# Kernel tuning notes

Measured on AMD Instinct MI355X. Metric: run time of the kernel, lower is better.

Reference implementation:

```python
import jax, jax.numpy as jnp
import numpy as np

M_SIZE = 128          # local window half-size
SCALING = 1.0 / np.sqrt(64.0)


def _window_allowed(seq_len, m):
    """Boolean [L, L] mask; True where attention is allowed.

    Matches torch window_mask: window width = 2m+1; rows near the edges are
    clamped so every row sees exactly `2m+1` columns.
    """
    size = 2 * m + 1
    if seq_len <= size:
        return jnp.ones((seq_len, seq_len), dtype=bool)
    rows = jnp.arange(seq_len)[:, None]            # [L,1]
    cols = jnp.arange(seq_len)[None, :]            # [1,L]
    start = jnp.clip(rows - m, 0, seq_len - size)  # [L,1]
    return (cols >= start) & (cols < start + size)


def setup_inputs() -> dict:
    key = jax.random.key(0)
    kq, kk, kv = jax.random.split(key, 3)
    B, L, D = 8, 4096, 64
    q = jax.random.normal(kq, (B, L, D), dtype=jnp.float32)
    k = jax.random.normal(kk, (B, L, D), dtype=jnp.float32)
    v = jax.random.normal(kv, (B, L, D), dtype=jnp.float32)
    return {"q": q, "k": k, "v": v}


def reference(q, k, v):
    # scores: [B, Lq, Lk]
    scores = jnp.einsum("bqd,bkd->bqk", q, k) * SCALING
    allowed = _window_allowed(q.shape[1], M_SIZE)          # [L, L]
    scores = jnp.where(allowed[None, :, :], scores, -jnp.inf)
    attention = jax.nn.softmax(scores, axis=2)
    out = jnp.einsum("bqk,bkv->bqv", attention, v)
    return (out, attention)
```

## Files before the change

### kernel.cpp

```cpp
#include <hip/hip_runtime.h>
#include <math.h>

#define L_SEQ 4096
#define D_HEAD 64
#define M_WIN 128
#define WIN 257
#define QB 8
#define W 264
#define WF4 66
#define ATTS 272
#define SCALE 0.125f

#define RL(v, i) __uint_as_float(__builtin_amdgcn_readlane(__float_as_uint(v), (i)))

static __device__ __forceinline__ unsigned bfr(float x) {
    unsigned u = __float_as_uint(x);
    return (u + 0x7fffu + ((u >> 16) & 1u)) >> 16;
}
static __device__ __forceinline__ unsigned bfpack(float lo, float hi) {
    return bfr(lo) | (bfr(hi) << 16);
}

__global__ __launch_bounds__(256, 3) void win_attn_kernel(
    const float* __restrict__ Q, const float* __restrict__ K,
    const float* __restrict__ V, float* __restrict__ OutO,
    float* __restrict__ OutA)
{
    extern __shared__ float smem[];
    uint4* k_su = (uint4*)smem;
    float* att  = smem + 2112 * 4;

    const int t  = threadIdx.x;
    const int w  = t >> 6;
    const int ln = t & 63;

    const int bid = (blockIdx.x & 7) * 512 + (blockIdx.x >> 3);
    const int b   = bid >> 9;
    const int q0  = (bid & 511) * QB;

    int s0 = q0 - M_WIN;
    if (s0 < 0) s0 = 0;
    if (s0 > L_SEQ - WIN) s0 = L_SEQ - WIN;
    const int wcount = (L_SEQ - s0 < W) ? (L_SEQ - s0) : W;

    {
        const float4* Kg = (const float4*)(K + ((size_t)(b * L_SEQ + s0)) * D_HEAD);
        #pragma unroll 3
        for (int idx = t; idx < 264 * 8; idx += 256) {
            int row = idx >> 3, c8 = idx & 7;
            int gr  = (row < wcount) ? row : wcount - 1;
            float4 a  = Kg[(size_t)gr * 16 + c8 * 2];
            float4 bb = Kg[(size_t)gr * 16 + c8 * 2 + 1];
            uint4 d;
            d.x = bfpack(a.x, a.y);   d.y = bfpack(a.z, a.w);
            d.z = bfpack(bb.x, bb.y); d.w = bfpack(bb.z, bb.w);
            k_su[row * 8 + (c8 ^ (row & 7))] = d;
        }
    }
    const int r0g = q0 + 2 * w;
    const float qv0 = Q[((size_t)(b * L_SEQ) + r0g)     * D_HEAD + ln];
    const float qv1 = Q[((size_t)(b * L_SEQ) + r0g + 1) * D_HEAD + ln];
    if (ln < 16) {
        int r = 2 * w + (ln >> 3);
        att[r * ATTS + 264 + (ln & 7)] = 0.f;
    }
    __syncthreads();

    float p0[5], p1[5];
    {
        const uint4* kp[5];
        int msk[5];
        #pragma unroll
        for (int cg = 0; cg < 5; ++cg) {
            int colr = cg * 64 + ln;
            int col  = (colr < W) ? colr : W - 1;
            kp[cg]  = k_su + (size_t)col * 8;
            msk[cg] = col & 7;
            p0[cg] = 0.f; p1[cg] = 0.f;
        }
        #pragma unroll
        for (int c8 = 0; c8 < 8; ++c8) {
            float a0 = RL(qv0, 8*c8+0), a1 = RL(qv0, 8*c8+1),
                  a2 = RL(qv0, 8*c8+2), a3 = RL(qv0, 8*c8+3),
                  a4 = RL(qv0, 8*c8+4), a5 = RL(qv0, 8*c8+5),
                  a6 = RL(qv0, 8*c8+6), a7 = RL(qv0, 8*c8+7);
            float b0 = RL(qv1, 8*c8+0), b1 = RL(qv1, 8*c8+1),
                  b2 = RL(qv1, 8*c8+2), b3 = RL(qv1, 8*c8+3),
                  b4 = RL(qv1, 8*c8+4), b5 = RL(qv1, 8*c8+5),
                  b6 = RL(qv1, 8*c8+6), b7 = RL(qv1, 8*c8+7);
            #pragma unroll
            for (int cg = 0; cg < 5; ++cg) {
                uint4 kk = kp[cg][c8 ^ msk[cg]];
                float e0 = __uint_as_float(kk.x << 16);
                float e1 = __uint_as_float(kk.x & 0xffff0000u);
                float e2 = __uint_as_float(kk.y << 16);
                float e3 = __uint_as_float(kk.y & 0xffff0000u);
                float e4 = __uint_as_float(kk.z << 16);
                float e5 = __uint_as_float(kk.z & 0xffff0000u);
                float e6 = __uint_as_float(kk.w << 16);
                float e7 = __uint_as_float(kk.w & 0xffff0000u);
                p0[cg] += a0*e0 + a1*e1 + a2*e2 + a3*e3
                        + a4*e4 + a5*e5 + a6*e6 + a7*e7;
                p1[cg] += b0*e0 + b1*e1 + b2*e2 + b3*e3
                        + b4*e4 + b5*e5 + b6*e6 + b7*e7;
            }
        }
        #pragma unroll
        for (int cg = 0; cg < 5; ++cg) { p0[cg] *= SCALE; p1[cg] *= SCALE; }
    }

    {
        int st0 = r0g - M_WIN;
        if (st0 < 0) st0 = 0;
        if (st0 > L_SEQ - WIN) st0 = L_SEQ - WIN;
        const int lo0 = st0 - s0;
        int st1 = r0g + 1 - M_WIN;
        if (st1 < 0) st1 = 0;
        if (st1 > L_SEQ - WIN) st1 = L_SEQ - WIN;
        const int lo1 = st1 - s0;

        float m0 = -1e30f, m1 = -1e30f;
        #pragma unroll
        for (int cg = 0; cg < 5; ++cg) {
            int colr = cg * 64 + ln;
            bool in0 = (colr >= lo0) && (colr < lo0 + WIN);
            bool in1 = (colr >= lo1) && (colr < lo1 + WIN);
            p0[cg] = in0 ? p0[cg] : -1e30f;
            p1[cg] = in1 ? p1[cg] : -1e30f;
            m0 = fmaxf(m0, p0[cg]);
            m1 = fmaxf(m1, p1[cg]);
        }
        #pragma unroll
        for (int off = 32; off >= 1; off >>= 1) {
            m0 = fmaxf(m0, __shfl_xor(m0, off));
            m1 = fmaxf(m1, __shfl_xor(m1, off));
        }
        float sum0 = 0.f, sum1 = 0.f;
        #pragma unroll
        for (int cg = 0; cg < 5; ++cg) {
            float e0 = (p0[cg] <= -1e29f) ? 0.f : __expf(p0[cg] - m0);
            float e1 = (p1[cg] <= -1e29f) ? 0.f : __expf(p1[cg] - m1);
            p0[cg] = e0; p1[cg] = e1;
            sum0 += e0; sum1 += e1;
        }
        #pragma unroll
        for (int off = 32; off >= 1; off >>= 1) {
            sum0 += __shfl_xor(sum0, off);
            sum1 += __shfl_xor(sum1, off);
        }
        const float inv0 = 1.f / sum0, inv1 = 1.f / sum1;
        #pragma unroll
        for (int cg = 0; cg < 5; ++cg) {
            int colr = cg * 64 + ln;
            if (colr < W) {
                att[(2 * w)     * ATTS + colr] = p0[cg] * inv0;
                att[(2 * w + 1) * ATTS + colr] = p1[cg] * inv1;
            }
        }
    }

    {
        const int cq = ln >> 4;
        const int dg = ln & 15;
        const float4* Vg4 = (const float4*)(V + ((size_t)(b * L_SEQ + s0)) * D_HEAD);
        const float4* a4r0 = (const float4*)(att + (2 * w) * ATTS);
        const float4* a4r1 = (const float4*)(att + (2 * w + 1) * ATTS);
        float4 acc0 = {0.f,0.f,0.f,0.f}, acc1 = {0.f,0.f,0.f,0.f};
        #pragma unroll 2
        for (int G = 0; G < 17; ++G) {
            float4 pa = a4r0[4 * G + cq];
            float4 pb = a4r1[4 * G + cq];
            #pragma unroll
            for (int e = 0; e < 4; ++e) {
                int col  = 16 * G + 4 * cq + e;
                int colc = (col < wcount) ? col : wcount - 1;
                float4 vv = Vg4[(size_t)colc * 16 + dg];
                float fa = (e == 0) ? pa.x : (e == 1) ? pa.y : (e == 2) ? pa.z : pa.w;
                float fb = (e == 0) ? pb.x : (e == 1) ? pb.y : (e == 2) ? pb.z : pb.w;
                acc0.x += fa * vv.x; acc0.y += fa * vv.y;
                acc0.z += fa * vv.z; acc0.w += fa * vv.w;
                acc1.x += fb * vv.x; acc1.y += fb * vv.y;
                acc1.z += fb * vv.z; acc1.w += fb * vv.w;
            }
        }
        #pragma unroll
        for (int off = 16; off <= 32; off <<= 1) {
            acc0.x += __shfl_xor(acc0.x, off); acc0.y += __shfl_xor(acc0.y, off);
            acc0.z += __shfl_xor(acc0.z, off); acc0.w += __shfl_xor(acc0.w, off);
            acc1.x += __shfl_xor(acc1.x, off); acc1.y += __shfl_xor(acc1.y, off);
            acc1.z += __shfl_xor(acc1.z, off); acc1.w += __shfl_xor(acc1.w, off);
        }
        if (ln < 16) {
            float4* o4 = (float4*)(OutO + ((size_t)(b * L_SEQ + r0g)) * D_HEAD);
            o4[dg]      = acc0;
            o4[16 + dg] = acc1;
        }
    }

    if ((s0 & 3) == 0) {
        const int zlo = s0 >> 2;
        #pragma unroll
        for (int r = 0; r < 2; ++r) {
            float4* rowp = (float4*)(OutA + ((size_t)(b * L_SEQ + r0g + r)) * L_SEQ);
            const float4* arow = (const float4*)(att + (2 * w + r) * ATTS);
            #pragma unroll 4
            for (int j = 0; j < 16; ++j) {
                int f4i = j * 64 + ln;
                int u4  = f4i - zlo;
                float4 wv = {0.f,0.f,0.f,0.f};
                if (u4 >= 0 && u4 < WF4) wv = arow[u4];
                rowp[f4i] = wv;
            }
        }
    } else {
        #pragma unroll
        for (int r = 0; r < 2; ++r) {
            float4* rowp = (float4*)(OutA + ((size_t)(b * L_SEQ + r0g + r)) * L_SEQ);
            const float* arow = att + (2 * w + r) * ATTS;
            #pragma unroll 2
            for (int j = 0; j < 16; ++j) {
                int f4i = j * 64 + ln;
                int u   = 4 * f4i - s0;
                float4 wv;
                wv.x = (u     >= 0 && u     < W) ? arow[u]     : 0.f;
                wv.y = (u + 1 >= 0 && u + 1 < W) ? arow[u + 1] : 0.f;
                wv.z = (u + 2 >= 0 && u + 2 < W) ? arow[u + 2] : 0.f;
                wv.w = (u + 3 >= 0 && u + 3 < W) ? arow[u + 3] : 0.f;
                rowp[f4i] = wv;
            }
        }
    }
}

extern "C" void kernel_launch(void* const* d_in, const int* in_sizes, int n_in,
                              void* d_out, int out_size, void* d_ws, size_t ws_size,
                              hipStream_t stream) {
    const float* Q = (const float*)d_in[0];
    const float* K = (const float*)d_in[1];
    const float* V = (const float*)d_in[2];
    float* OutO = (float*)d_out;
    float* OutA = OutO + (size_t)8 * L_SEQ * D_HEAD;

    const int smem_bytes = 2112 * 16 + QB * ATTS * 4;
    hipFuncSetAttribute((const void*)win_attn_kernel,
                        hipFuncAttributeMaxDynamicSharedMemorySize, smem_bytes);

    dim3 grid(8 * (L_SEQ / QB));
    dim3 block(256);
    win_attn_kernel<<<grid, block, smem_bytes, stream>>>(Q, K, V, OutO, OutA);
}
```

Before: 169.3 us.

## Split attention-matrix zero fill into dedicated blocks separate from windowed compute

```diff
diff --git a/kernel.cpp b/kernel.cpp
--- a/kernel.cpp
+++ b/kernel.cpp
@@ -30,13 +30,35 @@
     uint4* k_su = (uint4*)smem;
     float* att  = smem + 2112 * 4;
 
+    const int braw = blockIdx.x;
+    const int mod  = braw % 3;
+
+    if (mod == 2) {
+        const int fid = braw / 3;
+        const float4 z = {0.f, 0.f, 0.f, 0.f};
+        #pragma unroll 1
+        for (int rr = 0; rr < 16; ++rr) {
+            int grow = fid * 16 + rr;
+            int qg   = grow & (L_SEQ - 1);
+            int q0   = qg & ~(QB - 1);
+            int s0   = q0 - M_WIN;
+            if (s0 < 0) s0 = 0;
+            if (s0 > L_SEQ - WIN) s0 = L_SEQ - WIN;
+            const int zlo = s0 >> 2;
+            const int zhi = (s0 & 3) ? 1024 : zlo + WF4;
+            float4* rowp = (float4*)(OutA + (size_t)grow * L_SEQ);
+            for (int i = threadIdx.x; i < zlo; i += 256)      rowp[i] = z;
+            for (int i = zhi + threadIdx.x; i < 1024; i += 256) rowp[i] = z;
+        }
+        return;
+    }
+
+    const int cid = (braw / 3) * 2 + mod;
     const int t  = threadIdx.x;
     const int w  = t >> 6;
     const int ln = t & 63;
-
-    const int bid = (blockIdx.x & 7) * 512 + (blockIdx.x >> 3);
-    const int b   = bid >> 9;
-    const int q0  = (bid & 511) * QB;
+    const int b   = cid >> 9;
+    const int q0  = (cid & 511) * QB;
 
     int s0 = q0 - M_WIN;
     if (s0 < 0) s0 = 0;
@@ -203,23 +225,16 @@
         for (int r = 0; r < 2; ++r) {
             float4* rowp = (float4*)(OutA + ((size_t)(b * L_SEQ + r0g + r)) * L_SEQ);
             const float4* arow = (const float4*)(att + (2 * w + r) * ATTS);
-            #pragma unroll 4
-            for (int j = 0; j < 16; ++j) {
-                int f4i = j * 64 + ln;
-                int u4  = f4i - zlo;
-                float4 wv = {0.f,0.f,0.f,0.f};
-                if (u4 >= 0 && u4 < WF4) wv = arow[u4];
-                rowp[f4i] = wv;
-            }
+            for (int i = ln; i < WF4; i += 64)
+                rowp[zlo + i] = arow[i];
         }
     } else {
         #pragma unroll
         for (int r = 0; r < 2; ++r) {
             float4* rowp = (float4*)(OutA + ((size_t)(b * L_SEQ + r0g + r)) * L_SEQ);
             const float* arow = att + (2 * w + r) * ATTS;
-            #pragma unroll 2
-            for (int j = 0; j < 16; ++j) {
-                int f4i = j * 64 + ln;
+            for (int i = ln; i < 65; i += 64) {
+                int f4i = 959 + i;
                 int u   = 4 * f4i - s0;
                 float4 wv;
                 wv.x = (u     >= 0 && u     < W) ? arow[u]     : 0.f;
@@ -245,7 +260,7 @@
     hipFuncSetAttribute((const void*)win_attn_kernel,
                         hipFuncAttributeMaxDynamicSharedMemorySize, smem_bytes);
 
-    dim3 grid(8 * (L_SEQ / QB));
+    dim3 grid(6144);
     dim3 block(256);
     win_attn_kernel<<<grid, block, smem_bytes, stream>>>(Q, K, V, OutO, OutA);
 }
```

Measured after the change: 183.9 us. +8.7%, slower.
